# Performance work log

Hardware: AMD Instinct MI355X
Metric: run time of the kernel (lower is better)

## Reference

```python
import jax, jax.numpy as jnp
import numpy as np

IN_CHANNELS = 8
OUT_CHANNELS = 32
KERNEL_SIZE = 5
BATCH = 16
H = W = 128


def setup_inputs() -> dict:
    key = jax.random.key(0)
    k_in, k_hit, k_miss = jax.random.split(key, 3)
    x = jax.random.normal(k_in, (BATCH, IN_CHANNELS, H, W), dtype=jnp.float32)
    stdv = 1.0 / np.sqrt(IN_CHANNELS * KERNEL_SIZE ** 2)
    K_hit = jax.random.uniform(k_hit, (OUT_CHANNELS, IN_CHANNELS, KERNEL_SIZE, KERNEL_SIZE),
                               minval=-stdv, maxval=stdv, dtype=jnp.float32)
    K_miss = jax.random.uniform(k_miss, (OUT_CHANNELS, IN_CHANNELS, KERNEL_SIZE, KERNEL_SIZE),
                                minval=-stdv, maxval=stdv, dtype=jnp.float32)
    return {"input": x, "K_hit": K_hit, "K_miss": K_miss}


def _hitmiss(x, K_hit, K_miss):
    # x: [B,C,H,W]; K_*: [O,C,k,k]
    # out[b,o,y,x] = min_{c,u,v}(x[b,c,y+u,x+v] - K_hit[o,c,u,v])
    #             - max_{c,u,v}(x[b,c,y+u,x+v] - K_miss[o,c,u,v])
    # (torch code computes F_hit = maxpool(-(patch - K_hit)) so -F_hit = min(patch - K_hit),
    #  F_miss = maxpool(patch - K_miss); output = -F_hit - F_miss.)
    B, C, Hh, Ww = x.shape
    O, _, k, _ = K_hit.shape
    fh = Hh - k + 1
    hit_min = jnp.full((B, O, fh, fh), jnp.inf, dtype=x.dtype)
    miss_max = jnp.full((B, O, fh, fh), -jnp.inf, dtype=x.dtype)
    for u in range(k):  # fixed small loop over kernel offsets (k*k = 25)
        for v in range(k):
            win = x[:, :, u:u + fh, v:v + fh]          # [B,C,fh,fh]
            win_b = win[:, None]                        # [B,1,C,fh,fh]
            dh = win_b - K_hit[None, :, :, u, v, None, None]   # [B,O,C,fh,fh]
            dm = win_b - K_miss[None, :, :, u, v, None, None]
            hit_min = jnp.minimum(hit_min, dh.min(axis=2))
            miss_max = jnp.maximum(miss_max, dm.max(axis=2))
    return hit_min - miss_max


def reference(input, K_hit, K_miss):
    return _hitmiss(input, K_hit, K_miss)
```

## Files before the change

### kernel.cpp

```cpp
#include <hip/hip_runtime.h>
#include <math.h>

constexpr int IC   = 8;
constexpr int OC   = 32;
constexpr int KS   = 5;
constexpr int B_   = 16;
constexpr int HW_  = 128;
constexpr int FH   = 124;
constexpr int KTAP = KS * KS;
constexpr int OG   = 4;
constexpr int OPG  = 8;
constexpr int ROWS = 4;

typedef _Float16 h2 __attribute__((ext_vector_type(2)));

__global__ void pack_k_kernel(const float* __restrict__ Kh,
                              const float* __restrict__ Km,
                              unsigned* __restrict__ Kpk) {
    int idx = blockIdx.x * 256 + threadIdx.x;
    if (idx >= IC * OG * KTAP * 2 * OPG) return;
    int oi = idx & 7;
    int h  = (idx >> 3) & 1;
    int t  = (idx >> 4) % KTAP;
    int cg = (idx >> 4) / KTAP;
    int g  = cg & (OG - 1), c = cg >> 2;
    int o  = g * OPG + oi;
    const float* K = h ? Km : Kh;
    float k = -K[(o * IC + c) * KTAP + t];
    _Float16 nk = (_Float16)k;
    unsigned short us = __builtin_bit_cast(unsigned short, nk);
    Kpk[idx] = (unsigned)us | ((unsigned)us << 16);
}

__global__ __launch_bounds__(256, 8) void hitmiss_f16_kernel(
    const float* __restrict__ x,
    const unsigned* __restrict__ Kpk,
    float* __restrict__ out)
{
    const int lane = threadIdx.x & 63;
    const int wid  = threadIdx.x >> 6;
    const int i = blockIdx.x * ROWS + wid;
    const int b = blockIdx.y, g = blockIdx.z;
    const int j0 = lane * 2;
    if (j0 >= FH) return;

    h2 hit[OPG], miss[OPG];
    const h2 pinf = {(_Float16)INFINITY, (_Float16)INFINITY};
    const h2 ninf = {(_Float16)(-INFINITY), (_Float16)(-INFINITY)};
#pragma unroll
    for (int oi = 0; oi < OPG; ++oi) { hit[oi] = pinf; miss[oi] = ninf; }

#pragma unroll 1
    for (int c = 0; c < IC; ++c) {
        const float* xp = x + (((b * IC + c) * HW_) + i) * HW_ + j0;
        h2 xpk[KTAP];
#pragma unroll
        for (int u = 0; u < KS; ++u) {
            const float2 f0 = *(const float2*)(xp + u * HW_);
            const float2 f1 = *(const float2*)(xp + u * HW_ + 2);
            const float2 f2 = *(const float2*)(xp + u * HW_ + 4);
            const float fv[6] = {f0.x, f0.y, f1.x, f1.y, f2.x, f2.y};
#pragma unroll
            for (int v = 0; v < KS; ++v)
                xpk[u * KS + v] = __builtin_bit_cast(h2,
                    __builtin_amdgcn_cvt_pkrtz(fv[v], fv[v + 1]));
        }
        const unsigned* kc = Kpk + (size_t)((c * OG + g) * KTAP) * 2 * OPG;
#pragma unroll
        for (int t = 0; t < KTAP; ++t) {
#pragma unroll
            for (int oi = 0; oi < OPG; ++oi) {
                const h2 nh = __builtin_bit_cast(h2, kc[t * 16 + oi]);
                const h2 nm = __builtin_bit_cast(h2, kc[t * 16 + 8 + oi]);
                hit[oi]  = __builtin_elementwise_min(xpk[t] + nh, hit[oi]);
                miss[oi] = __builtin_elementwise_max(xpk[t] + nm, miss[oi]);
            }
        }
    }

#pragma unroll
    for (int oi = 0; oi < OPG; ++oi) {
        const h2 r = hit[oi] - miss[oi];
        const int o = g * OPG + oi;
        float* op = out + (((size_t)b * OC + o) * FH + i) * FH + j0;
        op[0] = (float)r[0];
        op[1] = (float)r[1];
    }
}

__global__ __launch_bounds__(128) void hitmiss_f32_kernel(
    const float* __restrict__ x,
    const float* __restrict__ Kh,
    const float* __restrict__ Km,
    float* __restrict__ out)
{
    const int j = threadIdx.x;
    const int i = blockIdx.x;
    const int b = blockIdx.y;
    if (j >= FH) return;

    float hit[OC], miss[OC];
#pragma unroll
    for (int o = 0; o < OC; ++o) { hit[o] = INFINITY; miss[o] = -INFINITY; }

#pragma unroll 1
    for (int c = 0; c < IC; ++c) {
        const float* xp = x + (((b * IC + c) * HW_) + i) * HW_ + j;
        float xw[KTAP];
#pragma unroll
        for (int u = 0; u < KS; ++u)
#pragma unroll
            for (int v = 0; v < KS; ++v)
                xw[u * KS + v] = xp[u * HW_ + v];
#pragma unroll
        for (int t = 0; t < KTAP - 1; t += 2) {
            const float x0 = xw[t], x1 = xw[t + 1];
#pragma unroll
            for (int o = 0; o < OC; ++o) {
                const float kh0 = Kh[(o * IC + c) * KTAP + t];
                const float kh1 = Kh[(o * IC + c) * KTAP + t + 1];
                const float km0 = Km[(o * IC + c) * KTAP + t];
                const float km1 = Km[(o * IC + c) * KTAP + t + 1];
                hit[o]  = fminf(fminf(x0 - kh0, x1 - kh1), hit[o]);
                miss[o] = fmaxf(fmaxf(x0 - km0, x1 - km1), miss[o]);
            }
        }
        {
            const float x0 = xw[KTAP - 1];
#pragma unroll
            for (int o = 0; o < OC; ++o) {
                hit[o]  = fminf(hit[o],  x0 - Kh[(o * IC + c) * KTAP + KTAP - 1]);
                miss[o] = fmaxf(miss[o], x0 - Km[(o * IC + c) * KTAP + KTAP - 1]);
            }
        }
    }

    float* op = out + ((size_t)(b * OC) * FH + i) * FH + j;
#pragma unroll
    for (int o = 0; o < OC; ++o)
        op[(size_t)o * FH * FH] = hit[o] - miss[o];
}

extern "C" void kernel_launch(void* const* d_in, const int* in_sizes, int n_in,
                              void* d_out, int out_size, void* d_ws, size_t ws_size,
                              hipStream_t stream) {
    const float* x  = (const float*)d_in[0];
    const float* Kh = (const float*)d_in[1];
    const float* Km = (const float*)d_in[2];
    float* out = (float*)d_out;

    const size_t kdwords = (size_t)IC * OG * KTAP * 2 * OPG;
    if (ws_size >= kdwords * sizeof(unsigned)) {
        unsigned* Kpk = (unsigned*)d_ws;
        pack_k_kernel<<<(int)((kdwords + 255) / 256), 256, 0, stream>>>(Kh, Km, Kpk);
        dim3 grid(FH / ROWS, B_, OG);
        hitmiss_f16_kernel<<<grid, 256, 0, stream>>>(x, Kpk, out);
    } else {
        dim3 grid(FH, B_);
        hitmiss_f32_kernel<<<grid, 128, 0, stream>>>(x, Kh, Km, out);
    }
}
```

Measured before the change: 172.6 us.

## Compute two output rows per thread to reuse kernel loads and input rows

Each wave now produces two adjacent output rows, loading KS+1 input rows once and reusing every packed kernel value across both rows. This halves the per-output cost of the scalar kernel-weight loads and input conversion. Outputs are written with a float2 store instead of two scalar stores. Register pressure doubles for the accumulators, so the occupancy hint drops to 4 blocks per CU. The grid of 16 row blocks over-covers the 124 rows, and a guard discards the extra waves.

```diff
diff --git a/kernel.cpp b/kernel.cpp
--- a/kernel.cpp
+++ b/kernel.cpp
@@ -10,7 +10,6 @@
 constexpr int KTAP = KS * KS;
 constexpr int OG   = 4;
 constexpr int OPG  = 8;
-constexpr int ROWS = 4;
 
 typedef _Float16 h2 __attribute__((ext_vector_type(2)));
 
@@ -32,59 +31,69 @@
     Kpk[idx] = (unsigned)us | ((unsigned)us << 16);
 }
 
-__global__ __launch_bounds__(256, 8) void hitmiss_f16_kernel(
+__global__ __launch_bounds__(256, 4) void hitmiss_f16_kernel(
     const float* __restrict__ x,
     const unsigned* __restrict__ Kpk,
     float* __restrict__ out)
 {
     const int lane = threadIdx.x & 63;
     const int wid  = threadIdx.x >> 6;
-    const int i = blockIdx.x * ROWS + wid;
+    const int i0 = blockIdx.x * 8 + wid * 2;
     const int b = blockIdx.y, g = blockIdx.z;
     const int j0 = lane * 2;
-    if (j0 >= FH) return;
+    if (j0 >= FH || i0 >= FH) return;
 
-    h2 hit[OPG], miss[OPG];
+    h2 hit[2][OPG], miss[2][OPG];
     const h2 pinf = {(_Float16)INFINITY, (_Float16)INFINITY};
     const h2 ninf = {(_Float16)(-INFINITY), (_Float16)(-INFINITY)};
 #pragma unroll
-    for (int oi = 0; oi < OPG; ++oi) { hit[oi] = pinf; miss[oi] = ninf; }
+    for (int r = 0; r < 2; ++r)
+#pragma unroll
+        for (int oi = 0; oi < OPG; ++oi) { hit[r][oi] = pinf; miss[r][oi] = ninf; }
 
 #pragma unroll 1
     for (int c = 0; c < IC; ++c) {
-        const float* xp = x + (((b * IC + c) * HW_) + i) * HW_ + j0;
-        h2 xpk[KTAP];
+        const float* xp = x + (((b * IC + c) * HW_) + i0) * HW_ + j0;
+        h2 xq[KS + 1][KS];
 #pragma unroll
-        for (int u = 0; u < KS; ++u) {
-            const float2 f0 = *(const float2*)(xp + u * HW_);
-            const float2 f1 = *(const float2*)(xp + u * HW_ + 2);
-            const float2 f2 = *(const float2*)(xp + u * HW_ + 4);
+        for (int r = 0; r < KS + 1; ++r) {
+            const float2 f0 = *(const float2*)(xp + r * HW_);
+            const float2 f1 = *(const float2*)(xp + r * HW_ + 2);
+            const float2 f2 = *(const float2*)(xp + r * HW_ + 4);
             const float fv[6] = {f0.x, f0.y, f1.x, f1.y, f2.x, f2.y};
 #pragma unroll
             for (int v = 0; v < KS; ++v)
-                xpk[u * KS + v] = __builtin_bit_cast(h2,
+                xq[r][v] = __builtin_bit_cast(h2,
                     __builtin_amdgcn_cvt_pkrtz(fv[v], fv[v + 1]));
         }
         const unsigned* kc = Kpk + (size_t)((c * OG + g) * KTAP) * 2 * OPG;
 #pragma unroll
-        for (int t = 0; t < KTAP; ++t) {
+        for (int u = 0; u < KS; ++u) {
 #pragma unroll
-            for (int oi = 0; oi < OPG; ++oi) {
-                const h2 nh = __builtin_bit_cast(h2, kc[t * 16 + oi]);
-                const h2 nm = __builtin_bit_cast(h2, kc[t * 16 + 8 + oi]);
-                hit[oi]  = __builtin_elementwise_min(xpk[t] + nh, hit[oi]);
-                miss[oi] = __builtin_elementwise_max(xpk[t] + nm, miss[oi]);
+            for (int v = 0; v < KS; ++v) {
+                const int t = u * KS + v;
+#pragma unroll
+                for (int oi = 0; oi < OPG; ++oi) {
+                    const h2 nh = __builtin_bit_cast(h2, kc[t * 16 + oi]);
+                    const h2 nm = __builtin_bit_cast(h2, kc[t * 16 + 8 + oi]);
+                    hit[0][oi]  = __builtin_elementwise_min(xq[u][v]     + nh, hit[0][oi]);
+                    hit[1][oi]  = __builtin_elementwise_min(xq[u + 1][v] + nh, hit[1][oi]);
+                    miss[0][oi] = __builtin_elementwise_max(xq[u][v]     + nm, miss[0][oi]);
+                    miss[1][oi] = __builtin_elementwise_max(xq[u + 1][v] + nm, miss[1][oi]);
+                }
             }
         }
     }
 
 #pragma unroll
+    for (int r = 0; r < 2; ++r)
+#pragma unroll
     for (int oi = 0; oi < OPG; ++oi) {
-        const h2 r = hit[oi] - miss[oi];
+        const h2 res = hit[r][oi] - miss[r][oi];
         const int o = g * OPG + oi;
-        float* op = out + (((size_t)b * OC + o) * FH + i) * FH + j0;
-        op[0] = (float)r[0];
-        op[1] = (float)r[1];
+        float* op = out + (((size_t)b * OC + o) * FH + (i0 + r)) * FH + j0;
+        float2 st; st.x = (float)res[0]; st.y = (float)res[1];
+        *(float2*)op = st;
     }
 }
 
@@ -153,7 +162,7 @@
     if (ws_size >= kdwords * sizeof(unsigned)) {
         unsigned* Kpk = (unsigned*)d_ws;
         pack_k_kernel<<<(int)((kdwords + 255) / 256), 256, 0, stream>>>(Kh, Km, Kpk);
-        dim3 grid(FH / ROWS, B_, OG);
+        dim3 grid(16, B_, OG);
         hitmiss_f16_kernel<<<grid, 256, 0, stream>>>(x, Kpk, out);
     } else {
         dim3 grid(FH, B_);
```

Result: no change. 172.8 us (+0.1%).
